# Kernel tuning notes

Hardware: AMD Instinct MI355X
Metric: run time of the kernel (lower is better)

The kernel has to match this reference:

```python
import jax, jax.numpy as jnp
import numpy as np

B, LQ, LK, D = 8, 2048, 2048, 1024


def setup_inputs() -> dict:
    key = jax.random.key(0)
    k1, k2, k3, k4, k5 = jax.random.split(key, 5)
    inp = jax.random.normal(k1, (B, LQ, D), dtype=jnp.float32)
    memory = jax.random.normal(k2, (B, LK, D), dtype=jnp.float32)
    # 0/1 float mask over memory positions (1 = masked out)
    mask = (jax.random.uniform(k3, (B, LK)) < 0.15).astype(jnp.float32)
    # nn.Linear(D, 1, bias=False): weight shape [1, D], kaiming-uniform-ish init
    w_input = jax.random.uniform(k4, (1, D), dtype=jnp.float32,
                                 minval=-1.0 / np.sqrt(D), maxval=1.0 / np.sqrt(D))
    # dot_scale ~ U(0, 1/sqrt(D)) per original .uniform_(1/input_size**0.5)
    dot_scale = jax.random.uniform(k5, (D,), dtype=jnp.float32,
                                   minval=0.0, maxval=1.0 / np.sqrt(D))
    return {"input": inp, "memory": memory, "mask": mask,
            "w_input": w_input, "dot_scale": dot_scale}


def reference(input, memory, mask, w_input, dot_scale):
    # input_dot: Linear(D,1,bias=False) -> [B, Lq, 1]
    input_dot = jnp.einsum('bqd,od->bqo', input, w_input)  # o == 1
    # cross_dot: (input * dot_scale) @ memory^T -> [B, Lq, Lk]
    cross_dot = jnp.einsum('bqd,bkd->bqk', input * dot_scale, memory)
    att = input_dot + cross_dot - 1e30 * mask[:, None, :]
    weight_one = jax.nn.softmax(att, axis=-1)  # [B, Lq, Lk]
    output_one = jnp.einsum('bqk,bkd->bqd', weight_one, memory)
    return output_one
```

## Files before the change

### kernel.cpp

```cpp
#include <hip/hip_runtime.h>

#define B_  8
#define LQ_ 2048
#define LK_ 2048
#define D_  1024

typedef unsigned short u16;
using short8  = __attribute__((ext_vector_type(8))) short;
using floatx4 = __attribute__((ext_vector_type(4))) float;

#define GAS __attribute__((address_space(1)))
#define LAS __attribute__((address_space(3)))

__device__ __forceinline__ u16 f2bf(float f) {
  unsigned u = __float_as_uint(f);
  u += 0x7fffu + ((u >> 16) & 1u);
  return (u16)(u >> 16);
}
__device__ __forceinline__ float bf2f(u16 h) {
  return __uint_as_float(((unsigned)h) << 16);
}

__global__ void prep(const float* __restrict__ in, const float* __restrict__ mem,
                     const float* __restrict__ ds, u16* __restrict__ qb,
                     u16* __restrict__ mb, u16* __restrict__ mbT,
                     float* __restrict__ denom) {
  __shared__ u16 tile[64][68];
  int tid = threadIdx.x;
  int tx = tid & 15, ty = tid >> 4;
  int b = blockIdx.z;

  if (denom && blockIdx.y == 16 && blockIdx.x == 0 && blockIdx.z == 0) {
    float4 z = {0.f, 0.f, 0.f, 0.f};
    float4* d4 = (float4*)denom;
#pragma unroll
    for (int i = 0; i < (B_ * LQ_ / 4) / 256; i++)
      d4[tid + i * 256] = z;
  }

  if (blockIdx.y < 16) {
    int k0 = blockIdx.x * 64, d0 = blockIdx.y * 64;
    const float* mB = mem + (size_t)b * LK_ * D_;
    u16* mbB = mb  + (size_t)b * LK_ * D_;
    u16* mtB = mbT + (size_t)b * D_ * LK_;
#pragma unroll
    for (int i = 0; i < 4; i++) {
      int r = ty + 16 * i;
      float4 v = *(const float4*)(mB + (size_t)(k0 + r) * D_ + d0 + tx * 4);
      ushort4 h;
      h.x = f2bf(v.x); h.y = f2bf(v.y); h.z = f2bf(v.z); h.w = f2bf(v.w);
      *(ushort4*)(mbB + (size_t)(k0 + r) * D_ + d0 + tx * 4) = h;
      *(ushort4*)(&tile[r][tx * 4]) = h;
    }
    __syncthreads();
#pragma unroll
    for (int i = 0; i < 4; i++) {
      int rr = ty + 16 * i;
      ushort4 o;
      o.x = tile[tx * 4 + 0][rr];
      o.y = tile[tx * 4 + 1][rr];
      o.z = tile[tx * 4 + 2][rr];
      o.w = tile[tx * 4 + 3][rr];
      *(ushort4*)(mtB + (size_t)(d0 + rr) * LK_ + k0 + tx * 4) = o;
    }
  } else {
    int q0 = blockIdx.x * 64, d0 = (blockIdx.y - 16) * 64;
    const float* iB = in + (size_t)b * LQ_ * D_;
    u16* qB = qb + (size_t)b * LQ_ * D_;
    float4 s4 = *(const float4*)(ds + d0 + tx * 4);
#pragma unroll
    for (int i = 0; i < 4; i++) {
      int r = ty + 16 * i;
      float4 v = *(const float4*)(iB + (size_t)(q0 + r) * D_ + d0 + tx * 4);
      ushort4 h;
      h.x = f2bf(v.x * s4.x); h.y = f2bf(v.y * s4.y);
      h.z = f2bf(v.z * s4.z); h.w = f2bf(v.w * s4.w);
      *(ushort4*)(qB + (size_t)(q0 + r) * D_ + d0 + tx * 4) = h;
    }
  }
}

template <int MODE>
__global__ void gemm_bt(const u16* __restrict__ A, const u16* __restrict__ Bm,
                        void* __restrict__ C, const float* __restrict__ mask,
                        float* __restrict__ denom,
                        int K, int ld, int ldc,
                        size_t sA, size_t sB, size_t sC) {
  __shared__ __align__(16) u16 As[128 * 64];
  __shared__ __align__(16) u16 Bs[128 * 64];
  int tid = threadIdx.x;
  int lane = tid & 63, w = tid >> 6;
  int wm = (w >> 1) * 64, wn = (w & 1) * 64;
  int lm = lane & 15, quad = lane >> 4;

  int tiles_n = gridDim.x;
  int bid = (blockIdx.z * gridDim.y + blockIdx.y) * tiles_n + blockIdx.x;
  int bz = bid & 7;
  int s = bid >> 3;
  const int GM = 8;
  int per_group = GM * tiles_n;
  int group = s / per_group;
  int rem = s - group * per_group;
  int tm = group * GM + (rem & (GM - 1));
  int tn = rem >> 3;

  const u16* Ab = A  + (size_t)bz * sA + (size_t)(tm * 128) * ld;
  const u16* Bb = Bm + (size_t)bz * sB + (size_t)(tn * 128) * ld;

  size_t goff[4];
  u16 *lA[4], *lB[4];
#pragma unroll
  for (int j = 0; j < 4; j++) {
    int c = tid + 256 * j;
    int half = c >> 9;
    int row = (c & 511) >> 2;
    int ko = half * 32 + (c & 3) * 8;
    goff[j] = (size_t)row * ld + ko;
    lA[j] = As + c * 8;
    lB[j] = Bs + c * 8;
  }

  floatx4 acc[4][4];
#pragma unroll
  for (int mi = 0; mi < 4; mi++)
#pragma unroll
    for (int ni = 0; ni < 4; ni++)
      acc[mi][ni] = {0.f, 0.f, 0.f, 0.f};

  float rs[4] = {0.f, 0.f, 0.f, 0.f};

  for (int k0 = 0; k0 < K; k0 += 64) {
#pragma unroll
    for (int j = 0; j < 4; j++) {
      __builtin_amdgcn_global_load_lds((GAS void*)(Ab + goff[j] + k0),
                                       (LAS void*)lA[j], 16, 0, 0);
      __builtin_amdgcn_global_load_lds((GAS void*)(Bb + goff[j] + k0),
                                       (LAS void*)lB[j], 16, 0, 0);
    }
    __syncthreads();

#pragma unroll
    for (int kk = 0; kk < 2; kk++) {
      const u16* Ah = As + kk * 4096;
      const u16* Bh = Bs + kk * 4096;
      short8 af[4], bf[4];
#pragma unroll
      for (int mi = 0; mi < 4; mi++)
        af[mi] = *(const short8*)(Ah + ((wm + mi * 16 + lm) << 5) + (quad << 3));
#pragma unroll
      for (int ni = 0; ni < 4; ni++)
        bf[ni] = *(const short8*)(Bh + ((wn + ni * 16 + lm) << 5) + (quad << 3));

      if constexpr (MODE == 2) {
#pragma unroll
        for (int mi = 0; mi < 4; mi++) {
          uint4 u = *(const uint4*)&af[mi];
          rs[mi] += __uint_as_float(u.x << 16) + __uint_as_float(u.x & 0xffff0000u)
                  + __uint_as_float(u.y << 16) + __uint_as_float(u.y & 0xffff0000u)
                  + __uint_as_float(u.z << 16) + __uint_as_float(u.z & 0xffff0000u)
                  + __uint_as_float(u.w << 16) + __uint_as_float(u.w & 0xffff0000u);
        }
      }

#pragma unroll
      for (int mi = 0; mi < 4; mi++)
#pragma unroll
        for (int ni = 0; ni < 4; ni++)
          acc[mi][ni] = __builtin_amdgcn_mfma_f32_16x16x32_bf16(af[mi], bf[ni],
                                                                acc[mi][ni], 0, 0, 0);
    }
    __syncthreads();
  }

  int gm0 = tm * 128 + wm + quad * 4;
  int gn0 = tn * 128 + wn + lm;
  size_t cb = (size_t)bz * sC;

  if constexpr (MODE == 1) {
    const float* mrow = mask + (size_t)bz * LK_;
    bool msk[4];
#pragma unroll
    for (int ni = 0; ni < 4; ni++) msk[ni] = (mrow[gn0 + ni * 16] != 0.0f);
#pragma unroll
    for (int mi = 0; mi < 4; mi++) {
#pragma unroll
      for (int r = 0; r < 4; r++) {
        int row = gm0 + mi * 16 + r;
        size_t rowoff = cb + (size_t)row * ldc + gn0;
        float part = 0.f;
#pragma unroll
        for (int ni = 0; ni < 4; ni++) {
          float e = msk[ni] ? 0.f : __expf(acc[mi][ni][r]);
          u16 h = f2bf(e);
          ((u16*)C)[rowoff + ni * 16] = h;
          part += bf2f(h);
        }
        if (denom) {
          part += __shfl_xor(part, 1, 64);
          part += __shfl_xor(part, 2, 64);
          part += __shfl_xor(part, 4, 64);
          part += __shfl_xor(part, 8, 64);
          if (lm == 0) atomicAdd(&denom[(size_t)bz * LQ_ + row], part);
        }
      }
    }
  } else if constexpr (MODE == 0) {
#pragma unroll
    for (int mi = 0; mi < 4; mi++) {
#pragma unroll
      for (int r = 0; r < 4; r++) {
        int row = gm0 + mi * 16 + r;
        float is = 1.0f / denom[(size_t)bz * LQ_ + row];
        size_t rowoff = cb + (size_t)row * ldc + gn0;
#pragma unroll
        for (int ni = 0; ni < 4; ni++)
          ((float*)C)[rowoff + ni * 16] = acc[mi][ni][r] * is;
      }
    }
  } else {
    float inv[4];
#pragma unroll
    for (int mi = 0; mi < 4; mi++) {
      rs[mi] += __shfl_xor(rs[mi], 16, 64);
      rs[mi] += __shfl_xor(rs[mi], 32, 64);
      inv[mi] = 1.0f / rs[mi];
    }
#pragma unroll
    for (int mi = 0; mi < 4; mi++) {
#pragma unroll
      for (int r = 0; r < 4; r++) {
        size_t rowoff = cb + (size_t)(gm0 + mi * 16 + r) * ldc + gn0;
        float is = __shfl(inv[mi], quad * 4 + r, 64);
#pragma unroll
        for (int ni = 0; ni < 4; ni++)
          ((float*)C)[rowoff + ni * 16] = acc[mi][ni][r] * is;
      }
    }
  }
}

extern "C" void kernel_launch(void* const* d_in, const int* in_sizes, int n_in,
                              void* d_out, int out_size, void* d_ws, size_t ws_size,
                              hipStream_t stream) {
  const float* input  = (const float*)d_in[0];
  const float* memory = (const float*)d_in[1];
  const float* mask   = (const float*)d_in[2];
  const float* dscale = (const float*)d_in[4];

  char* ws = (char*)d_ws;
  u16* qb  = (u16*)(ws);
  u16* mb  = (u16*)(ws + (size_t)32 * 1024 * 1024);
  u16* mbT = (u16*)(ws + (size_t)64 * 1024 * 1024);
  u16* E   = (u16*)(ws + (size_t)96 * 1024 * 1024);
  size_t base = (size_t)160 * 1024 * 1024;
  bool have_denom = ws_size >= base + (size_t)B_ * LQ_ * sizeof(float);
  float* denom = have_denom ? (float*)(ws + base) : nullptr;
  float* out = (float*)d_out;

  hipLaunchKernelGGL(prep, dim3(32, 32, B_), dim3(256), 0, stream,
                     input, memory, dscale, qb, mb, mbT, denom);
  hipLaunchKernelGGL((gemm_bt<1>), dim3(LK_ / 128, LQ_ / 128, B_), dim3(256), 0,
                     stream, qb, mb, (void*)E, mask, denom, D_, D_, LK_,
                     (size_t)LQ_ * D_, (size_t)LK_ * D_, (size_t)LQ_ * LK_);
  if (have_denom)
    hipLaunchKernelGGL((gemm_bt<0>), dim3(D_ / 128, LQ_ / 128, B_), dim3(256), 0,
                       stream, E, mbT, (void*)out, nullptr, denom, LK_, LK_, D_,
                       (size_t)LQ_ * LK_, (size_t)D_ * LK_, (size_t)LQ_ * D_);
  else
    hipLaunchKernelGGL((gemm_bt<2>), dim3(D_ / 128, LQ_ / 128, B_), dim3(256), 0,
                       stream, E, mbT, (void*)out, nullptr, nullptr, LK_, LK_, D_,
                       (size_t)LQ_ * LK_, (size_t)D_ * LK_, (size_t)LQ_ * D_);
}
```

Baseline: 333.4 us.

## Enlarge GEMM tiles to 256x256 with double-buffered LDS pipeline and swizzle

Rewrites the bf16 MFMA GEMM kernel to use 256x256 block tiles with 512 threads (8 waves, each 128x64), double-buffering LDS planes so the next k-tile's global-to-LDS loads overlap the current MFMAs via explicit vmcnt waits and barriers. It adds an XOR swizzle on LDS slots to reduce bank conflicts and raises wave priority around the MFMA sections. Grouped tile ordering changes from 8 to 4. This aims to improve arithmetic intensity and hide memory latency, at the cost of 128 KiB of LDS per block and higher register pressure, which may limit occupancy.

```diff
diff --git a/kernel.cpp b/kernel.cpp
--- a/kernel.cpp
+++ b/kernel.cpp
@@ -81,100 +81,135 @@
 }
 
 template <int MODE>
-__global__ void gemm_bt(const u16* __restrict__ A, const u16* __restrict__ Bm,
-                        void* __restrict__ C, const float* __restrict__ mask,
-                        float* __restrict__ denom,
-                        int K, int ld, int ldc,
-                        size_t sA, size_t sB, size_t sC) {
-  __shared__ __align__(16) u16 As[128 * 64];
-  __shared__ __align__(16) u16 Bs[128 * 64];
-  int tid = threadIdx.x;
-  int lane = tid & 63, w = tid >> 6;
-  int wm = (w >> 1) * 64, wn = (w & 1) * 64;
-  int lm = lane & 15, quad = lane >> 4;
-
-  int tiles_n = gridDim.x;
+__global__ __launch_bounds__(512, 2) void gemm_bt(
+    const u16* __restrict__ A, const u16* __restrict__ Bm,
+    void* __restrict__ C, const float* __restrict__ mask,
+    float* __restrict__ denom, int K, int ld, int ldc,
+    size_t sA, size_t sB, size_t sC) {
+  __shared__ __align__(16) u16 As[4 * 8192];
+  __shared__ __align__(16) u16 Bs[4 * 8192];
+
+  const int tid = threadIdx.x;
+  const int lane = tid & 63, w = tid >> 6;
+  const int lm = lane & 15, quad = (lane >> 4) & 3;
+  const int wm = (w >> 2) * 128, wn = (w & 3) * 64;
+
+  const int tiles_n = gridDim.x;
   int bid = (blockIdx.z * gridDim.y + blockIdx.y) * tiles_n + blockIdx.x;
   int bz = bid & 7;
   int s = bid >> 3;
-  const int GM = 8;
+  const int GM = 4;
   int per_group = GM * tiles_n;
   int group = s / per_group;
   int rem = s - group * per_group;
   int tm = group * GM + (rem & (GM - 1));
-  int tn = rem >> 3;
-
-  const u16* Ab = A  + (size_t)bz * sA + (size_t)(tm * 128) * ld;
-  const u16* Bb = Bm + (size_t)bz * sB + (size_t)(tn * 128) * ld;
-
-  size_t goff[4];
-  u16 *lA[4], *lB[4];
-#pragma unroll
-  for (int j = 0; j < 4; j++) {
-    int c = tid + 256 * j;
-    int half = c >> 9;
-    int row = (c & 511) >> 2;
-    int ko = half * 32 + (c & 3) * 8;
-    goff[j] = (size_t)row * ld + ko;
-    lA[j] = As + c * 8;
-    lB[j] = Bs + c * 8;
-  }
-
-  floatx4 acc[4][4];
-#pragma unroll
-  for (int mi = 0; mi < 4; mi++)
-#pragma unroll
-    for (int ni = 0; ni < 4; ni++)
-      acc[mi][ni] = {0.f, 0.f, 0.f, 0.f};
-
-  float rs[4] = {0.f, 0.f, 0.f, 0.f};
-
-  for (int k0 = 0; k0 < K; k0 += 64) {
-#pragma unroll
-    for (int j = 0; j < 4; j++) {
-      __builtin_amdgcn_global_load_lds((GAS void*)(Ab + goff[j] + k0),
-                                       (LAS void*)lA[j], 16, 0, 0);
-      __builtin_amdgcn_global_load_lds((GAS void*)(Bb + goff[j] + k0),
-                                       (LAS void*)lB[j], 16, 0, 0);
-    }
-    __syncthreads();
-
-#pragma unroll
-    for (int kk = 0; kk < 2; kk++) {
-      const u16* Ah = As + kk * 4096;
-      const u16* Bh = Bs + kk * 4096;
-      short8 af[4], bf[4];
-#pragma unroll
-      for (int mi = 0; mi < 4; mi++)
-        af[mi] = *(const short8*)(Ah + ((wm + mi * 16 + lm) << 5) + (quad << 3));
-#pragma unroll
-      for (int ni = 0; ni < 4; ni++)
-        bf[ni] = *(const short8*)(Bh + ((wn + ni * 16 + lm) << 5) + (quad << 3));
-
-      if constexpr (MODE == 2) {
-#pragma unroll
-        for (int mi = 0; mi < 4; mi++) {
-          uint4 u = *(const uint4*)&af[mi];
-          rs[mi] += __uint_as_float(u.x << 16) + __uint_as_float(u.x & 0xffff0000u)
-                  + __uint_as_float(u.y << 16) + __uint_as_float(u.y & 0xffff0000u)
-                  + __uint_as_float(u.z << 16) + __uint_as_float(u.z & 0xffff0000u)
-                  + __uint_as_float(u.w << 16) + __uint_as_float(u.w & 0xffff0000u);
-        }
-      }
-
-#pragma unroll
-      for (int mi = 0; mi < 4; mi++)
-#pragma unroll
-        for (int ni = 0; ni < 4; ni++)
-          acc[mi][ni] = __builtin_amdgcn_mfma_f32_16x16x32_bf16(af[mi], bf[ni],
-                                                                acc[mi][ni], 0, 0, 0);
-    }
-    __syncthreads();
-  }
-
-  int gm0 = tm * 128 + wm + quad * 4;
-  int gn0 = tn * 128 + wn + lm;
-  size_t cb = (size_t)bz * sC;
+  int tn = rem >> 2;
+
+  const u16* Ab = A  + (size_t)bz * sA + (size_t)(tm * 256) * ld;
+  const u16* Bb = Bm + (size_t)bz * sB + (size_t)(tn * 256) * ld;
+
+  int goff[2], ldst[2];
+#pragma unroll
+  for (int j = 0; j < 2; j++) {
+    int c = tid + 512 * j;
+    int row = c >> 2;
+    int slot = (c & 3) ^ ((row >> 1) & 3);
+    goff[j] = row * ld + slot * 8;
+    ldst[j] = c * 8;
+  }
+
+  const int sw = quad ^ ((lm >> 1) & 3);
+  const int aoff = (wm + lm) * 32 + sw * 8;
+  const int boff = (wn + lm) * 32 + sw * 8;
+
+  auto stageA = [&](int koff, int plane) {
+#pragma unroll
+    for (int j = 0; j < 2; j++)
+      __builtin_amdgcn_global_load_lds((GAS void*)(Ab + goff[j] + koff),
+                                       (LAS void*)(As + (plane << 13) + ldst[j]),
+                                       16, 0, 0);
+  };
+  auto stageB = [&](int koff, int plane) {
+#pragma unroll
+    for (int j = 0; j < 2; j++)
+      __builtin_amdgcn_global_load_lds((GAS void*)(Bb + goff[j] + koff),
+                                       (LAS void*)(Bs + (plane << 13) + ldst[j]),
+                                       16, 0, 0);
+  };
+
+  floatx4 acc[8][4];
+#pragma unroll
+  for (int i = 0; i < 8; i++)
+#pragma unroll
+    for (int j = 0; j < 4; j++)
+      acc[i][j] = {0.f, 0.f, 0.f, 0.f};
+
+  float rs[8] = {0.f, 0.f, 0.f, 0.f, 0.f, 0.f, 0.f, 0.f};
+  short8 bf[4];
+
+#define DS_PHASE(MH, KK, CUR, STG)                                            \
+  {                                                                           \
+    const u16* Ap = As + (((CUR) * 2 + (KK)) << 13);                          \
+    if ((MH) == 0) {                                                          \
+      const u16* Bp = Bs + (((CUR) * 2 + (KK)) << 13);                        \
+      _Pragma("unroll")                                                       \
+      for (int ni = 0; ni < 4; ni++)                                          \
+        bf[ni] = *(const short8*)(Bp + boff + ni * 512);                      \
+    }                                                                         \
+    short8 af[4];                                                             \
+    _Pragma("unroll")                                                         \
+    for (int m = 0; m < 4; m++)                                               \
+      af[m] = *(const short8*)(Ap + aoff + ((MH) * 4 + m) * 512);             \
+    STG;                                                                      \
+    if constexpr (MODE == 2) {                                                \
+      _Pragma("unroll")                                                       \
+      for (int m = 0; m < 4; m++) {                                           \
+        uint4 u = *(const uint4*)&af[m];                                      \
+        rs[(MH) * 4 + m] +=                                                   \
+            __uint_as_float(u.x << 16) + __uint_as_float(u.x & 0xffff0000u)   \
+          + __uint_as_float(u.y << 16) + __uint_as_float(u.y & 0xffff0000u)   \
+          + __uint_as_float(u.z << 16) + __uint_as_float(u.z & 0xffff0000u)   \
+          + __uint_as_float(u.w << 16) + __uint_as_float(u.w & 0xffff0000u);  \
+      }                                                                       \
+    }                                                                         \
+    __builtin_amdgcn_s_setprio(1);                                            \
+    _Pragma("unroll")                                                         \
+    for (int m = 0; m < 4; m++)                                               \
+      _Pragma("unroll")                                                       \
+      for (int ni = 0; ni < 4; ni++)                                          \
+        acc[(MH) * 4 + m][ni] = __builtin_amdgcn_mfma_f32_16x16x32_bf16(      \
+            af[m], bf[ni], acc[(MH) * 4 + m][ni], 0, 0, 0);                   \
+    __builtin_amdgcn_s_setprio(0);                                            \
+  }
+
+  const int NT = K >> 6;
+  stageA(0, 0); stageB(0, 0); stageA(32, 1); stageB(32, 1);
+
+  for (int t = 0; t < NT; ++t) {
+    const int cur = t & 1, nb = cur ^ 1;
+    const bool have = (t + 1 < NT);
+    const int k0n = (t + 1) << 6;
+
+    asm volatile("s_waitcnt vmcnt(4)" ::: "memory");
+    __builtin_amdgcn_sched_barrier(0);
+    __builtin_amdgcn_s_barrier();
+
+    DS_PHASE(0, 0, cur, if (have) stageA(k0n, nb * 2))
+    DS_PHASE(1, 0, cur, if (have) stageB(k0n, nb * 2))
+
+    if (have) { asm volatile("s_waitcnt vmcnt(4)" ::: "memory"); }
+    else      { asm volatile("s_waitcnt vmcnt(0)" ::: "memory"); }
+    __builtin_amdgcn_sched_barrier(0);
+    __builtin_amdgcn_s_barrier();
+
+    DS_PHASE(0, 1, cur, if (have) stageA(k0n + 32, nb * 2 + 1))
+    DS_PHASE(1, 1, cur, if (have) stageB(k0n + 32, nb * 2 + 1))
+  }
+#undef DS_PHASE
+
+  const int gm0 = tm * 256 + wm + quad * 4;
+  const int gn0 = tn * 256 + wn + lm;
+  const size_t cb = (size_t)bz * sC;
 
   if constexpr (MODE == 1) {
     const float* mrow = mask + (size_t)bz * LK_;
@@ -182,7 +217,7 @@
 #pragma unroll
     for (int ni = 0; ni < 4; ni++) msk[ni] = (mrow[gn0 + ni * 16] != 0.0f);
 #pragma unroll
-    for (int mi = 0; mi < 4; mi++) {
+    for (int mi = 0; mi < 8; mi++) {
 #pragma unroll
       for (int r = 0; r < 4; r++) {
         int row = gm0 + mi * 16 + r;
@@ -206,7 +241,7 @@
     }
   } else if constexpr (MODE == 0) {
 #pragma unroll
-    for (int mi = 0; mi < 4; mi++) {
+    for (int mi = 0; mi < 8; mi++) {
 #pragma unroll
       for (int r = 0; r < 4; r++) {
         int row = gm0 + mi * 16 + r;
@@ -218,15 +253,15 @@
       }
     }
   } else {
-    float inv[4];
-#pragma unroll
-    for (int mi = 0; mi < 4; mi++) {
+    float inv[8];
+#pragma unroll
+    for (int mi = 0; mi < 8; mi++) {
       rs[mi] += __shfl_xor(rs[mi], 16, 64);
       rs[mi] += __shfl_xor(rs[mi], 32, 64);
       inv[mi] = 1.0f / rs[mi];
     }
 #pragma unroll
-    for (int mi = 0; mi < 4; mi++) {
+    for (int mi = 0; mi < 8; mi++) {
 #pragma unroll
       for (int r = 0; r < 4; r++) {
         size_t rowoff = cb + (size_t)(gm0 + mi * 16 + r) * ldc + gn0;
@@ -259,15 +294,15 @@
 
   hipLaunchKernelGGL(prep, dim3(32, 32, B_), dim3(256), 0, stream,
                      input, memory, dscale, qb, mb, mbT, denom);
-  hipLaunchKernelGGL((gemm_bt<1>), dim3(LK_ / 128, LQ_ / 128, B_), dim3(256), 0,
+  hipLaunchKernelGGL((gemm_bt<1>), dim3(LK_ / 256, LQ_ / 256, B_), dim3(512), 0,
                      stream, qb, mb, (void*)E, mask, denom, D_, D_, LK_,
                      (size_t)LQ_ * D_, (size_t)LK_ * D_, (size_t)LQ_ * LK_);
   if (have_denom)
-    hipLaunchKernelGGL((gemm_bt<0>), dim3(D_ / 128, LQ_ / 128, B_), dim3(256), 0,
+    hipLaunchKernelGGL((gemm_bt<0>), dim3(D_ / 256, LQ_ / 256, B_), dim3(512), 0,
                        stream, E, mbT, (void*)out, nullptr, denom, LK_, LK_, D_,
                        (size_t)LQ_ * LK_, (size_t)D_ * LK_, (size_t)LQ_ * D_);
   else
-    hipLaunchKernelGGL((gemm_bt<2>), dim3(D_ / 128, LQ_ / 128, B_), dim3(256), 0,
+    hipLaunchKernelGGL((gemm_bt<2>), dim3(D_ / 256, LQ_ / 256, B_), dim3(512), 0,
                        stream, E, mbT, (void*)out, nullptr, nullptr, LK_, LK_, D_,
                        (size_t)LQ_ * LK_, (size_t)D_ * LK_, (size_t)LQ_ * D_);
 }
```

After: 319.9 us. -4.1%, faster.
